# Performance work log

Measured on AMD Instinct MI355X. Metric: run time of the kernel, lower is better.

## Reference

```python
import jax, jax.numpy as jnp
import numpy as np

N = 50000
IN_DIM = 1024
HID = 64
HEADS = 4
OUT_DIM = 128
NEG_SLOPE = 0.2


def setup_inputs() -> dict:
    key = jax.random.key(0)
    ks = jax.random.split(key, 10)
    x = jax.random.normal(ks[0], (N, IN_DIM), dtype=jnp.float32)
    edge_index = jax.random.randint(ks[1], (2, 800000), 0, N, dtype=jnp.int64)
    # GATConv 1: input_dim -> hidden_dim, heads=HEADS, concat=True
    W1 = jax.random.normal(ks[2], (IN_DIM, HEADS * HID), dtype=jnp.float32) * (1.0 / np.sqrt(IN_DIM))
    att_src1 = jax.random.normal(ks[3], (HEADS, HID), dtype=jnp.float32) * 0.1
    att_dst1 = jax.random.normal(ks[4], (HEADS, HID), dtype=jnp.float32) * 0.1
    b1 = jnp.zeros((HEADS * HID,), dtype=jnp.float32)
    # GATConv 2: hidden_dim*heads -> output_dim, heads=1, concat=False
    W2 = jax.random.normal(ks[5], (HEADS * HID, OUT_DIM), dtype=jnp.float32) * (1.0 / np.sqrt(HEADS * HID))
    att_src2 = jax.random.normal(ks[6], (1, OUT_DIM), dtype=jnp.float32) * 0.1
    att_dst2 = jax.random.normal(ks[7], (1, OUT_DIM), dtype=jnp.float32) * 0.1
    b2 = jnp.zeros((OUT_DIM,), dtype=jnp.float32)
    return {"x": x, "edge_index": edge_index, "W1": W1, "att_src1": att_src1,
            "att_dst1": att_dst1, "b1": b1, "W2": W2, "att_src2": att_src2,
            "att_dst2": att_dst2, "b2": b2}


def _gat_conv(x, src, dst, W, a_src, a_dst, b, heads, concat):
    # x: [N, F_in]; src/dst: [E'] (self-loops already included)
    n = x.shape[0]
    h = (x @ W).reshape(n, heads, -1)                 # [N, H, D]
    # per-node attention halves (PyG style)
    alpha_s = jnp.sum(h * a_src[None], axis=-1)       # [N, H]
    alpha_d = jnp.sum(h * a_dst[None], axis=-1)       # [N, H]
    e = jax.nn.leaky_relu(alpha_s[src] + alpha_d[dst], NEG_SLOPE)  # [E', H]
    # segment softmax over incoming edges of each destination node
    m = jax.ops.segment_max(e, dst, num_segments=n)   # [N, H]
    m = jnp.where(jnp.isfinite(m), m, 0.0)
    e = jnp.exp(e - m[dst])
    s = jax.ops.segment_sum(e, dst, num_segments=n)   # [N, H]
    alpha = e / (s[dst] + 1e-16)                      # [E', H]
    out = jax.ops.segment_sum(h[src] * alpha[:, :, None], dst, num_segments=n)  # [N, H, D]
    out = out.reshape(n, -1) if concat else out.mean(axis=1)
    return out + b


def reference(x, edge_index, W1, att_src1, att_dst1, b1, W2, att_src2, att_dst2, b2):
    n = x.shape[0]
    # PyG GATConv default: add self-loops
    loops = jnp.arange(n, dtype=edge_index.dtype)
    src = jnp.concatenate([edge_index[0], loops])
    dst = jnp.concatenate([edge_index[1], loops])
    # dropout layers are identity in eval mode
    h = _gat_conv(x, src, dst, W1, att_src1, att_dst1, b1, HEADS, concat=True)
    h = jax.nn.elu(h)
    out = _gat_conv(h, src, dst, W2, att_src2, att_dst2, b2, 1, concat=False)
    # F.normalize(p=2, dim=-1)
    norm = jnp.maximum(jnp.linalg.norm(out, axis=-1, keepdims=True), 1e-12)
    return out / norm
```

## Files before the change

### kernel.cpp

```cpp
#include <hip/hip_runtime.h>
#include <math.h>

#define NNODES 50000
#define E0 800000
#define ETOT 850000
#define IN_DIM 1024
#define HEADS 4
#define C1 256
#define C2 128
#define NEG_SLOPE 0.2f

typedef short bf16x8 __attribute__((ext_vector_type(8)));
typedef float f32x4 __attribute__((ext_vector_type(4)));
typedef unsigned short ushort_t;

__device__ __forceinline__ void edge_sd(const int* __restrict__ ei, int e, int& s, int& d) {
    if (e < E0) { s = ei[e]; d = ei[E0 + e]; }
    else        { s = e - E0; d = s; }
}

__device__ __forceinline__ ushort_t f2b(float f) {
    unsigned u = __float_as_uint(f);
    return (ushort_t)((u + 0x7fffu + ((u >> 16) & 1u)) >> 16);
}
__device__ __forceinline__ float bf2f(ushort_t u) {
    return __uint_as_float((unsigned)u << 16);
}
__device__ __forceinline__ float lrelu(float v) { return v > 0.f ? v : NEG_SLOPE * v; }

__device__ __forceinline__ void gload_lds16(const void* g, void* l) {
    __builtin_amdgcn_global_load_lds(
        (const __attribute__((address_space(1))) unsigned int*)g,
        (__attribute__((address_space(3))) unsigned int*)l, 16, 0, 0);
}

__global__ __launch_bounds__(256) void wtrans_kernel(const float* __restrict__ W,
                                                     ushort_t* __restrict__ WT,
                                                     int K, int N)
{
    int idx = blockIdx.x * 256 + threadIdx.x;
    if (idx >= K * N) return;
    int k = idx / N, n = idx % N;
    WT[(size_t)n * K + k] = f2b(W[idx]);
}

__global__ __launch_bounds__(256) void gemm_fb(const float* __restrict__ A,
                                               const ushort_t* __restrict__ Bt,
                                               ushort_t* __restrict__ Cb,
                                               int M, int N, int K)
{
    __shared__ __align__(16) ushort_t As[4 * 128 * 8];
    __shared__ __align__(16) ushort_t Bs[4 * 128 * 8];

    const int tid  = threadIdx.x;
    const int lane = tid & 63;
    const int wid  = tid >> 6;
    const int wr   = wid >> 1, wc = wid & 1;
    const int rowBase = blockIdx.y * 128;
    const int colBase = blockIdx.x * 128;

    const int arow = tid >> 1;
    const int akh  = (tid & 1) * 2;
    const int aGRow = min(rowBase + arow, M - 1);
    const float* aptr = A + (size_t)aGRow * K + akh * 8;
    ushort_t* awr0 = &As[akh * 1024 + arow * 8];
    ushort_t* awr1 = awr0 + 1024;

    const ushort_t* bptr = Bt + (size_t)(colBase + lane) * K + wid * 8;
    ushort_t* bwr0 = &Bs[wid * 1024];
    ushort_t* bwr1 = bwr0 + 512;

    const int r0 = lane & 15;
    const int kh = lane >> 4;
    const ushort_t* ard = &As[kh * 1024 + (wr * 64 + r0) * 8];
    const ushort_t* brd = &Bs[kh * 1024 + (wc * 64 + r0) * 8];

    f32x4 zero = {0.f, 0.f, 0.f, 0.f};
    f32x4 acc[4][4];
    #pragma unroll
    for (int i = 0; i < 4; ++i)
        #pragma unroll
        for (int j = 0; j < 4; ++j) acc[i][j] = zero;

    for (int kt = 0; kt < K; kt += 32) {
        float4 f0 = *(const float4*)(aptr + kt + 0);
        float4 f1 = *(const float4*)(aptr + kt + 4);
        float4 f2 = *(const float4*)(aptr + kt + 8);
        float4 f3 = *(const float4*)(aptr + kt + 12);
        bf16x8 p0, p1;
        p0[0] = f2b(f0.x); p0[1] = f2b(f0.y); p0[2] = f2b(f0.z); p0[3] = f2b(f0.w);
        p0[4] = f2b(f1.x); p0[5] = f2b(f1.y); p0[6] = f2b(f1.z); p0[7] = f2b(f1.w);
        p1[0] = f2b(f2.x); p1[1] = f2b(f2.y); p1[2] = f2b(f2.z); p1[3] = f2b(f2.w);
        p1[4] = f2b(f3.x); p1[5] = f2b(f3.y); p1[6] = f2b(f3.z); p1[7] = f2b(f3.w);

        __syncthreads();
        *(bf16x8*)awr0 = p0;
        *(bf16x8*)awr1 = p1;
        gload_lds16(bptr + kt, bwr0);
        gload_lds16(bptr + (size_t)64 * K + kt, bwr1);
        __syncthreads();

        bf16x8 af[4], bfr[4];
        #pragma unroll
        for (int fi = 0; fi < 4; ++fi) af[fi] = *(const bf16x8*)(ard + fi * 128);
        #pragma unroll
        for (int fj = 0; fj < 4; ++fj) bfr[fj] = *(const bf16x8*)(brd + fj * 128);
        #pragma unroll
        for (int fi = 0; fi < 4; ++fi)
            #pragma unroll
            for (int fj = 0; fj < 4; ++fj)
                acc[fi][fj] = __builtin_amdgcn_mfma_f32_16x16x32_bf16(
                    af[fi], bfr[fj], acc[fi][fj], 0, 0, 0);
    }

    #pragma unroll
    for (int fi = 0; fi < 4; ++fi) {
        int row0 = rowBase + wr * 64 + fi * 16 + kh * 4;
        #pragma unroll
        for (int i = 0; i < 4; ++i) {
            int row = row0 + i;
            if (row < M) {
                #pragma unroll
                for (int fj = 0; fj < 4; ++fj)
                    Cb[(size_t)row * N + colBase + wc * 64 + fj * 16 + r0] = f2b(acc[fi][fj][i]);
            }
        }
    }
}

__global__ __launch_bounds__(256) void gemm_bb(const ushort_t* __restrict__ Ab,
                                               const ushort_t* __restrict__ Bt,
                                               ushort_t* __restrict__ Cb,
                                               int M, int N, int K)
{
    __shared__ __align__(16) ushort_t As[4 * 128 * 8];
    __shared__ __align__(16) ushort_t Bs[4 * 128 * 8];

    const int tid  = threadIdx.x;
    const int lane = tid & 63;
    const int wid  = tid >> 6;
    const int wr   = wid >> 1, wc = wid & 1;
    const int rowBase = blockIdx.y * 128;
    const int colBase = blockIdx.x * 128;

    const ushort_t* aptr0 = Ab + (size_t)min(rowBase + lane, M - 1) * K + wid * 8;
    const ushort_t* aptr1 = Ab + (size_t)min(rowBase + 64 + lane, M - 1) * K + wid * 8;
    ushort_t* awr0 = &As[wid * 1024];
    ushort_t* awr1 = awr0 + 512;

    const ushort_t* bptr = Bt + (size_t)(colBase + lane) * K + wid * 8;
    ushort_t* bwr0 = &Bs[wid * 1024];
    ushort_t* bwr1 = bwr0 + 512;

    const int r0 = lane & 15;
    const int kh = lane >> 4;
    const ushort_t* ard = &As[kh * 1024 + (wr * 64 + r0) * 8];
    const ushort_t* brd = &Bs[kh * 1024 + (wc * 64 + r0) * 8];

    f32x4 zero = {0.f, 0.f, 0.f, 0.f};
    f32x4 acc[4][4];
    #pragma unroll
    for (int i = 0; i < 4; ++i)
        #pragma unroll
        for (int j = 0; j < 4; ++j) acc[i][j] = zero;

    for (int kt = 0; kt < K; kt += 32) {
        __syncthreads();
        gload_lds16(aptr0 + kt, awr0);
        gload_lds16(aptr1 + kt, awr1);
        gload_lds16(bptr + kt, bwr0);
        gload_lds16(bptr + (size_t)64 * K + kt, bwr1);
        __syncthreads();

        bf16x8 af[4], bfr[4];
        #pragma unroll
        for (int fi = 0; fi < 4; ++fi) af[fi] = *(const bf16x8*)(ard + fi * 128);
        #pragma unroll
        for (int fj = 0; fj < 4; ++fj) bfr[fj] = *(const bf16x8*)(brd + fj * 128);
        #pragma unroll
        for (int fi = 0; fi < 4; ++fi)
            #pragma unroll
            for (int fj = 0; fj < 4; ++fj)
                acc[fi][fj] = __builtin_amdgcn_mfma_f32_16x16x32_bf16(
                    af[fi], bfr[fj], acc[fi][fj], 0, 0, 0);
    }

    #pragma unroll
    for (int fi = 0; fi < 4; ++fi) {
        int row0 = rowBase + wr * 64 + fi * 16 + kh * 4;
        #pragma unroll
        for (int i = 0; i < 4; ++i) {
            int row = row0 + i;
            if (row < M) {
                #pragma unroll
                for (int fj = 0; fj < 4; ++fj)
                    Cb[(size_t)row * N + colBase + wc * 64 + fj * 16 + r0] = f2b(acc[fi][fj][i]);
            }
        }
    }
}

__global__ __launch_bounds__(256) void alpha1_kernel(const ushort_t* __restrict__ h1b,
                                                     const float* __restrict__ asrc,
                                                     const float* __restrict__ adst,
                                                     float* __restrict__ out_s,
                                                     float* __restrict__ out_d)
{
    int n = blockIdx.x;
    int t = threadIdx.x;
    float h = bf2f(h1b[(size_t)n * C1 + t]);
    float s = h * asrc[t];
    float d = h * adst[t];
    #pragma unroll
    for (int off = 32; off > 0; off >>= 1) {
        s += __shfl_down(s, off);
        d += __shfl_down(d, off);
    }
    if ((t & 63) == 0) {
        out_s[n * HEADS + (t >> 6)] = s;
        out_d[n * HEADS + (t >> 6)] = d;
    }
}

__global__ __launch_bounds__(64) void alpha2_kernel(const ushort_t* __restrict__ h2b,
                                                    const float* __restrict__ asrc,
                                                    const float* __restrict__ adst,
                                                    float* __restrict__ out_s,
                                                    float* __restrict__ out_d)
{
    int n = blockIdx.x;
    int t = threadIdx.x;
    float a = bf2f(h2b[(size_t)n * C2 + t]);
    float b = bf2f(h2b[(size_t)n * C2 + t + 64]);
    float s = a * asrc[t] + b * asrc[t + 64];
    float d = a * adst[t] + b * adst[t + 64];
    #pragma unroll
    for (int off = 32; off > 0; off >>= 1) {
        s += __shfl_down(s, off);
        d += __shfl_down(d, off);
    }
    if (t == 0) { out_s[n] = s; out_d[n] = d; }
}

__global__ __launch_bounds__(256) void deg_kernel(const int* __restrict__ ei,
                                                  int* __restrict__ deg)
{
    int e = blockIdx.x * blockDim.x + threadIdx.x;
    if (e >= ETOT) return;
    int s, d; edge_sd(ei, e, s, d);
    atomicAdd(&deg[d], 1);
}

#define SCAN_T 1024
__global__ __launch_bounds__(SCAN_T) void scan_kernel(const int* __restrict__ deg,
                                                      int* __restrict__ rowptr)
{
    __shared__ int wsum[16];
    __shared__ int chunk_tot;
    __shared__ int carry_s;
    const int t = threadIdx.x, lane = t & 63, w = t >> 6;
    if (t == 0) carry_s = 0;
    __syncthreads();
    for (int base = 0; base < NNODES; base += SCAN_T * 4) {
        int idx = base + t * 4;
        int v0 = (idx + 0 < NNODES) ? deg[idx + 0] : 0;
        int v1 = (idx + 1 < NNODES) ? deg[idx + 1] : 0;
        int v2 = (idx + 2 < NNODES) ? deg[idx + 2] : 0;
        int v3 = (idx + 3 < NNODES) ? deg[idx + 3] : 0;
        int p0 = v0, p1 = p0 + v1, p2 = p1 + v2, p3 = p2 + v3;
        int incl = p3;
        #pragma unroll
        for (int off = 1; off < 64; off <<= 1) {
            int nb = __shfl_up(incl, off);
            if (lane >= off) incl += nb;
        }
        if (lane == 63) wsum[w] = incl;
        __syncthreads();
        if (w == 0 && lane < 16) {
            int ws = wsum[lane];
            int wincl = ws;
            #pragma unroll
            for (int off = 1; off < 16; off <<= 1) {
                int nb = __shfl_up(wincl, off);
                if (lane >= off) wincl += nb;
            }
            wsum[lane] = wincl - ws;
            if (lane == 15) chunk_tot = wincl;
        }
        __syncthreads();
        int carry = carry_s;
        int basev = carry + wsum[w] + (incl - p3);
        if (idx + 0 < NNODES) rowptr[idx + 0] = basev;
        if (idx + 1 < NNODES) rowptr[idx + 1] = basev + p0;
        if (idx + 2 < NNODES) rowptr[idx + 2] = basev + p1;
        if (idx + 3 < NNODES) rowptr[idx + 3] = basev + p2;
        __syncthreads();
        if (t == 0) carry_s = carry + chunk_tot;
        __syncthreads();
    }
    if (threadIdx.x == 0) rowptr[NNODES] = carry_s;
}

__global__ __launch_bounds__(256) void scatter_kernel(const int* __restrict__ ei,
                                                      int* __restrict__ cursor,
                                                      int* __restrict__ srcs)
{
    int e = blockIdx.x * blockDim.x + threadIdx.x;
    if (e >= ETOT) return;
    int s, d; edge_sd(ei, e, s, d);
    int pos = atomicAdd(&cursor[d], 1);
    srcs[pos] = s;
}

__global__ __launch_bounds__(256) void weights1_kernel(const int* __restrict__ rowptr,
                                                       const int* __restrict__ srcs,
                                                       const float4* __restrict__ as1,
                                                       const float4* __restrict__ ad1,
                                                       float4* __restrict__ wbuf)
{
    int d = blockIdx.x * 4 + (threadIdx.x >> 6);
    if (d >= NNODES) return;
    int lane = threadIdx.x & 63;
    int beg = rowptr[d], end = rowptr[d + 1];
    float4 adv = ad1[d];
    float m0 = -INFINITY, m1 = -INFINITY, m2 = -INFINITY, m3 = -INFINITY;
    for (int i = beg + lane; i < end; i += 64) {
        int s = srcs[i];
        float4 av = as1[s];
        m0 = fmaxf(m0, lrelu(av.x + adv.x));
        m1 = fmaxf(m1, lrelu(av.y + adv.y));
        m2 = fmaxf(m2, lrelu(av.z + adv.z));
        m3 = fmaxf(m3, lrelu(av.w + adv.w));
    }
    #pragma unroll
    for (int off = 32; off > 0; off >>= 1) {
        m0 = fmaxf(m0, __shfl_xor(m0, off));
        m1 = fmaxf(m1, __shfl_xor(m1, off));
        m2 = fmaxf(m2, __shfl_xor(m2, off));
        m3 = fmaxf(m3, __shfl_xor(m3, off));
    }
    float s0 = 0.f, s1 = 0.f, s2 = 0.f, s3 = 0.f;
    for (int i = beg + lane; i < end; i += 64) {
        int s = srcs[i];
        float4 av = as1[s];
        float w0 = expf(lrelu(av.x + adv.x) - m0);
        float w1 = expf(lrelu(av.y + adv.y) - m1);
        float w2 = expf(lrelu(av.z + adv.z) - m2);
        float w3 = expf(lrelu(av.w + adv.w) - m3);
        wbuf[i] = make_float4(w0, w1, w2, w3);
        s0 += w0; s1 += w1; s2 += w2; s3 += w3;
    }
    #pragma unroll
    for (int off = 32; off > 0; off >>= 1) {
        s0 += __shfl_xor(s0, off);
        s1 += __shfl_xor(s1, off);
        s2 += __shfl_xor(s2, off);
        s3 += __shfl_xor(s3, off);
    }
    float i0 = 1.f / (s0 + 1e-16f), i1 = 1.f / (s1 + 1e-16f);
    float i2 = 1.f / (s2 + 1e-16f), i3 = 1.f / (s3 + 1e-16f);
    for (int i = beg + lane; i < end; i += 64) {
        float4 wv = wbuf[i];
        wbuf[i] = make_float4(wv.x * i0, wv.y * i1, wv.z * i2, wv.w * i3);
    }
}

__global__ __launch_bounds__(256) void weights2_kernel(const int* __restrict__ rowptr,
                                                       const int* __restrict__ srcs,
                                                       const float* __restrict__ as2,
                                                       const float* __restrict__ ad2,
                                                       float* __restrict__ wbuf)
{
    int d = blockIdx.x * 4 + (threadIdx.x >> 6);
    if (d >= NNODES) return;
    int lane = threadIdx.x & 63;
    int beg = rowptr[d], end = rowptr[d + 1];
    float adv = ad2[d];
    float m = -INFINITY;
    for (int i = beg + lane; i < end; i += 64)
        m = fmaxf(m, lrelu(as2[srcs[i]] + adv));
    #pragma unroll
    for (int off = 32; off > 0; off >>= 1) m = fmaxf(m, __shfl_xor(m, off));
    float sm = 0.f;
    for (int i = beg + lane; i < end; i += 64) {
        float w = expf(lrelu(as2[srcs[i]] + adv) - m);
        wbuf[i] = w;
        sm += w;
    }
    #pragma unroll
    for (int off = 32; off > 0; off >>= 1) sm += __shfl_xor(sm, off);
    float inv = 1.f / (sm + 1e-16f);
    for (int i = beg + lane; i < end; i += 64) wbuf[i] *= inv;
}

__global__ __launch_bounds__(256) void aggr1_csr(const int* __restrict__ rowptr,
                                                 const int* __restrict__ srcs,
                                                 const ushort_t* __restrict__ h1b,
                                                 const float* __restrict__ wbuf,
                                                 const float* __restrict__ b1,
                                                 ushort_t* __restrict__ out)
{
    int d = blockIdx.x;
    int t = threadIdx.x;
    int head = t >> 6;
    int beg = rowptr[d], end = rowptr[d + 1];
    float acc = 0.f;
    int i = beg;
    for (; i + 1 < end; i += 2) {
        int s0 = srcs[i], s1 = srcs[i + 1];
        float a0 = wbuf[i * 4 + head], a1 = wbuf[i * 4 + 4 + head];
        float v0 = bf2f(h1b[(size_t)s0 * C1 + t]);
        float v1 = bf2f(h1b[(size_t)s1 * C1 + t]);
        acc = fmaf(a0, v0, acc);
        acc = fmaf(a1, v1, acc);
    }
    if (i < end) {
        int s0 = srcs[i];
        acc = fmaf(wbuf[i * 4 + head], bf2f(h1b[(size_t)s0 * C1 + t]), acc);
    }
    float o = acc + b1[t];
    out[(size_t)d * C1 + t] = f2b(o > 0.f ? o : (expf(o) - 1.f));
}

__global__ __launch_bounds__(128) void aggr2_csr(const int* __restrict__ rowptr,
                                                 const int* __restrict__ srcs,
                                                 const ushort_t* __restrict__ h2b,
                                                 const float* __restrict__ wbuf,
                                                 const float* __restrict__ b2,
                                                 float* __restrict__ out)
{
    int d = blockIdx.x;
    int t = threadIdx.x;
    int beg = rowptr[d], end = rowptr[d + 1];
    float acc = 0.f;
    int i = beg;
    for (; i + 1 < end; i += 2) {
        int s0 = srcs[i], s1 = srcs[i + 1];
        float a0 = wbuf[i], a1 = wbuf[i + 1];
        float v0 = bf2f(h2b[(size_t)s0 * C2 + t]);
        float v1 = bf2f(h2b[(size_t)s1 * C2 + t]);
        acc = fmaf(a0, v0, acc);
        acc = fmaf(a1, v1, acc);
    }
    if (i < end) acc = fmaf(wbuf[i], bf2f(h2b[(size_t)srcs[i] * C2 + t]), acc);
    float o = acc + b2[t];
    __shared__ float red[2];
    float sq = o * o;
    #pragma unroll
    for (int off = 32; off > 0; off >>= 1) sq += __shfl_down(sq, off);
    if ((t & 63) == 0) red[t >> 6] = sq;
    __syncthreads();
    float total = red[0] + red[1];
    float inv = 1.0f / fmaxf(sqrtf(total), 1e-12f);
    out[(size_t)d * C2 + t] = o * inv;
}

extern "C" void kernel_launch(void* const* d_in, const int* in_sizes, int n_in,
                              void* d_out, int out_size, void* d_ws, size_t ws_size,
                              hipStream_t stream)
{
    const float* x     = (const float*)d_in[0];
    const int*   ei    = (const int*)d_in[1];
    const float* W1    = (const float*)d_in[2];
    const float* asrc1 = (const float*)d_in[3];
    const float* adst1 = (const float*)d_in[4];
    const float* b1    = (const float*)d_in[5];
    const float* W2    = (const float*)d_in[6];
    const float* asrc2 = (const float*)d_in[7];
    const float* adst2 = (const float*)d_in[8];
    const float* b2    = (const float*)d_in[9];
    float* out = (float*)d_out;

    char* ws = (char*)d_ws;
    size_t off = 0;
    auto alloc = [&](size_t nbytes) {
        void* p = ws + off;
        off += (nbytes + 15) & ~(size_t)15;
        return p;
    };
    ushort_t* h1b    = (ushort_t*)alloc((size_t)NNODES * C1 * 2);
    ushort_t* act1b  = (ushort_t*)alloc((size_t)NNODES * C1 * 2);
    ushort_t* h2b    = (ushort_t*)alloc((size_t)NNODES * C2 * 2);
    ushort_t* W1T    = (ushort_t*)alloc((size_t)C1 * IN_DIM * 2);
    ushort_t* W2T    = (ushort_t*)alloc((size_t)C2 * C1 * 2);
    float*    as1    = (float*)alloc((size_t)NNODES * HEADS * 4);
    float*    ad1    = (float*)alloc((size_t)NNODES * HEADS * 4);
    float*    as2    = (float*)alloc((size_t)NNODES * 4);
    float*    ad2    = (float*)alloc((size_t)NNODES * 4);
    float*    wbuf1  = (float*)alloc((size_t)ETOT * HEADS * 4);
    float*    wbuf2  = (float*)alloc((size_t)ETOT * 4);
    int*      deg    = (int*)alloc((size_t)NNODES * 4);
    int*      rowptr = (int*)alloc((size_t)(NNODES + 1) * 4);
    int*      cursor = (int*)alloc((size_t)(NNODES + 1) * 4);
    int*      srcs   = (int*)alloc((size_t)ETOT * 4);

    const int eb = (ETOT + 255) / 256;
    const int nb4 = (NNODES + 3) / 4;

    wtrans_kernel<<<(IN_DIM * C1 + 255) / 256, 256, 0, stream>>>(W1, W1T, IN_DIM, C1);
    wtrans_kernel<<<(C1 * C2 + 255) / 256, 256, 0, stream>>>(W2, W2T, C1, C2);

    hipMemsetAsync(deg, 0, (size_t)NNODES * 4, stream);
    deg_kernel<<<eb, 256, 0, stream>>>(ei, deg);
    scan_kernel<<<1, SCAN_T, 0, stream>>>(deg, rowptr);
    hipMemcpyAsync(cursor, rowptr, (size_t)(NNODES + 1) * 4, hipMemcpyDeviceToDevice, stream);
    scatter_kernel<<<eb, 256, 0, stream>>>(ei, cursor, srcs);

    dim3 g1(C1 / 128, (NNODES + 127) / 128);
    gemm_fb<<<g1, 256, 0, stream>>>(x, W1T, h1b, NNODES, C1, IN_DIM);
    alpha1_kernel<<<NNODES, 256, 0, stream>>>(h1b, asrc1, adst1, as1, ad1);
    weights1_kernel<<<nb4, 256, 0, stream>>>(rowptr, srcs, (const float4*)as1,
                                             (const float4*)ad1, (float4*)wbuf1);
    aggr1_csr<<<NNODES, 256, 0, stream>>>(rowptr, srcs, h1b, wbuf1, b1, act1b);

    dim3 g2(C2 / 128, (NNODES + 127) / 128);
    gemm_bb<<<g2, 256, 0, stream>>>(act1b, W2T, h2b, NNODES, C2, C1);
    alpha2_kernel<<<NNODES, 64, 0, stream>>>(h2b, asrc2, adst2, as2, ad2);
    weights2_kernel<<<nb4, 256, 0, stream>>>(rowptr, srcs, as2, ad2, wbuf2);
    aggr2_csr<<<NNODES, 128, 0, stream>>>(rowptr, srcs, h2b, wbuf2, b2, out);
}
```

Baseline: 535.4 us.

## Double-buffer LDS tiles in both GEMM kernels to overlap loads with MFMA

Both GEMM kernels now keep two LDS buffers per operand. The next K-tile is prefetched into the idle buffer while MFMAs run on the current one, so each iteration needs one barrier instead of two. Launch bounds gain occupancy hints (3 and 4 blocks per CU). In exchange the kernels use twice the LDS and more registers, since the fp32 A prefetch values stay live across the MFMA block, which may cut occupancy.

```diff
diff --git a/kernel.cpp b/kernel.cpp
--- a/kernel.cpp
+++ b/kernel.cpp
@@ -44,13 +44,13 @@
     WT[(size_t)n * K + k] = f2b(W[idx]);
 }
 
-__global__ __launch_bounds__(256) void gemm_fb(const float* __restrict__ A,
-                                               const ushort_t* __restrict__ Bt,
-                                               ushort_t* __restrict__ Cb,
-                                               int M, int N, int K)
-{
-    __shared__ __align__(16) ushort_t As[4 * 128 * 8];
-    __shared__ __align__(16) ushort_t Bs[4 * 128 * 8];
+__global__ __launch_bounds__(256, 3) void gemm_fb(const float* __restrict__ A,
+                                                  const ushort_t* __restrict__ Bt,
+                                                  ushort_t* __restrict__ Cb,
+                                                  int M, int N, int K)
+{
+    __shared__ __align__(16) ushort_t As[2][4 * 128 * 8];
+    __shared__ __align__(16) ushort_t Bs[2][4 * 128 * 8];
 
     const int tid  = threadIdx.x;
     const int lane = tid & 63;
@@ -63,17 +63,17 @@
     const int akh  = (tid & 1) * 2;
     const int aGRow = min(rowBase + arow, M - 1);
     const float* aptr = A + (size_t)aGRow * K + akh * 8;
-    ushort_t* awr0 = &As[akh * 1024 + arow * 8];
-    ushort_t* awr1 = awr0 + 1024;
+    const int awoff0 = akh * 1024 + arow * 8;
+    const int awoff1 = awoff0 + 1024;
 
     const ushort_t* bptr = Bt + (size_t)(colBase + lane) * K + wid * 8;
-    ushort_t* bwr0 = &Bs[wid * 1024];
-    ushort_t* bwr1 = bwr0 + 512;
+    const int bwoff0 = wid * 1024;
+    const int bwoff1 = bwoff0 + 512;
 
     const int r0 = lane & 15;
     const int kh = lane >> 4;
-    const ushort_t* ard = &As[kh * 1024 + (wr * 64 + r0) * 8];
-    const ushort_t* brd = &Bs[kh * 1024 + (wc * 64 + r0) * 8];
+    const int ardoff = kh * 1024 + (wr * 64 + r0) * 8;
+    const int brdoff = kh * 1024 + (wc * 64 + r0) * 8;
 
     f32x4 zero = {0.f, 0.f, 0.f, 0.f};
     f32x4 acc[4][4];
@@ -82,35 +82,64 @@
         #pragma unroll
         for (int j = 0; j < 4; ++j) acc[i][j] = zero;
 
-    for (int kt = 0; kt < K; kt += 32) {
-        float4 f0 = *(const float4*)(aptr + kt + 0);
-        float4 f1 = *(const float4*)(aptr + kt + 4);
-        float4 f2 = *(const float4*)(aptr + kt + 8);
-        float4 f3 = *(const float4*)(aptr + kt + 12);
+    {
+        float4 f0 = *(const float4*)(aptr + 0);
+        float4 f1 = *(const float4*)(aptr + 4);
+        float4 f2 = *(const float4*)(aptr + 8);
+        float4 f3 = *(const float4*)(aptr + 12);
         bf16x8 p0, p1;
         p0[0] = f2b(f0.x); p0[1] = f2b(f0.y); p0[2] = f2b(f0.z); p0[3] = f2b(f0.w);
         p0[4] = f2b(f1.x); p0[5] = f2b(f1.y); p0[6] = f2b(f1.z); p0[7] = f2b(f1.w);
         p1[0] = f2b(f2.x); p1[1] = f2b(f2.y); p1[2] = f2b(f2.z); p1[3] = f2b(f2.w);
         p1[4] = f2b(f3.x); p1[5] = f2b(f3.y); p1[6] = f2b(f3.z); p1[7] = f2b(f3.w);
-
-        __syncthreads();
-        *(bf16x8*)awr0 = p0;
-        *(bf16x8*)awr1 = p1;
-        gload_lds16(bptr + kt, bwr0);
-        gload_lds16(bptr + (size_t)64 * K + kt, bwr1);
-        __syncthreads();
+        *(bf16x8*)&As[0][awoff0] = p0;
+        *(bf16x8*)&As[0][awoff1] = p1;
+        gload_lds16(bptr, &Bs[0][bwoff0]);
+        gload_lds16(bptr + (size_t)64 * K, &Bs[0][bwoff1]);
+    }
+    __syncthreads();
+
+    const ushort_t* rdA = As[0]; const ushort_t* rdB = Bs[0];
+    ushort_t*       stA = As[1]; ushort_t*       stB = Bs[1];
+
+    const int nt = K >> 5;
+    for (int t = 0; t < nt; ++t) {
+        const int kt = (t + 1) << 5;
+        const bool has_next = kt < K;
+        float4 f0, f1, f2, f3;
+        if (has_next) {
+            gload_lds16(bptr + kt, stB + bwoff0);
+            gload_lds16(bptr + (size_t)64 * K + kt, stB + bwoff1);
+            f0 = *(const float4*)(aptr + kt + 0);
+            f1 = *(const float4*)(aptr + kt + 4);
+            f2 = *(const float4*)(aptr + kt + 8);
+            f3 = *(const float4*)(aptr + kt + 12);
+        }
 
         bf16x8 af[4], bfr[4];
         #pragma unroll
-        for (int fi = 0; fi < 4; ++fi) af[fi] = *(const bf16x8*)(ard + fi * 128);
-        #pragma unroll
-        for (int fj = 0; fj < 4; ++fj) bfr[fj] = *(const bf16x8*)(brd + fj * 128);
+        for (int fi = 0; fi < 4; ++fi) af[fi] = *(const bf16x8*)(rdA + ardoff + fi * 128);
+        #pragma unroll
+        for (int fj = 0; fj < 4; ++fj) bfr[fj] = *(const bf16x8*)(rdB + brdoff + fj * 128);
         #pragma unroll
         for (int fi = 0; fi < 4; ++fi)
             #pragma unroll
             for (int fj = 0; fj < 4; ++fj)
                 acc[fi][fj] = __builtin_amdgcn_mfma_f32_16x16x32_bf16(
                     af[fi], bfr[fj], acc[fi][fj], 0, 0, 0);
+
+        if (has_next) {
+            bf16x8 p0, p1;
+            p0[0] = f2b(f0.x); p0[1] = f2b(f0.y); p0[2] = f2b(f0.z); p0[3] = f2b(f0.w);
+            p0[4] = f2b(f1.x); p0[5] = f2b(f1.y); p0[6] = f2b(f1.z); p0[7] = f2b(f1.w);
+            p1[0] = f2b(f2.x); p1[1] = f2b(f2.y); p1[2] = f2b(f2.z); p1[3] = f2b(f2.w);
+            p1[4] = f2b(f3.x); p1[5] = f2b(f3.y); p1[6] = f2b(f3.z); p1[7] = f2b(f3.w);
+            *(bf16x8*)(stA + awoff0) = p0;
+            *(bf16x8*)(stA + awoff1) = p1;
+        }
+        __syncthreads();
+        const ushort_t* tA = rdA; rdA = stA; stA = (ushort_t*)tA;
+        const ushort_t* tB = rdB; rdB = stB; stB = (ushort_t*)tB;
     }
 
     #pragma unroll
@@ -128,13 +157,13 @@
     }
 }
 
-__global__ __launch_bounds__(256) void gemm_bb(const ushort_t* __restrict__ Ab,
-                                               const ushort_t* __restrict__ Bt,
-                                               ushort_t* __restrict__ Cb,
-                                               int M, int N, int K)
-{
-    __shared__ __align__(16) ushort_t As[4 * 128 * 8];
-    __shared__ __align__(16) ushort_t Bs[4 * 128 * 8];
+__global__ __launch_bounds__(256, 4) void gemm_bb(const ushort_t* __restrict__ Ab,
+                                                  const ushort_t* __restrict__ Bt,
+                                                  ushort_t* __restrict__ Cb,
+                                                  int M, int N, int K)
+{
+    __shared__ __align__(16) ushort_t As[2][4 * 128 * 8];
+    __shared__ __align__(16) ushort_t Bs[2][4 * 128 * 8];
 
     const int tid  = threadIdx.x;
     const int lane = tid & 63;
@@ -145,17 +174,14 @@
 
     const ushort_t* aptr0 = Ab + (size_t)min(rowBase + lane, M - 1) * K + wid * 8;
     const ushort_t* aptr1 = Ab + (size_t)min(rowBase + 64 + lane, M - 1) * K + wid * 8;
-    ushort_t* awr0 = &As[wid * 1024];
-    ushort_t* awr1 = awr0 + 512;
-
-    const ushort_t* bptr = Bt + (size_t)(colBase + lane) * K + wid * 8;
-    ushort_t* bwr0 = &Bs[wid * 1024];
-    ushort_t* bwr1 = bwr0 + 512;
+    const ushort_t* bptr  = Bt + (size_t)(colBase + lane) * K + wid * 8;
+    const int woff0 = wid * 1024;
+    const int woff1 = woff0 + 512;
 
     const int r0 = lane & 15;
     const int kh = lane >> 4;
-    const ushort_t* ard = &As[kh * 1024 + (wr * 64 + r0) * 8];
-    const ushort_t* brd = &Bs[kh * 1024 + (wc * 64 + r0) * 8];
+    const int ardoff = kh * 1024 + (wr * 64 + r0) * 8;
+    const int brdoff = kh * 1024 + (wc * 64 + r0) * 8;
 
     f32x4 zero = {0.f, 0.f, 0.f, 0.f};
     f32x4 acc[4][4];
@@ -164,25 +190,40 @@
         #pragma unroll
         for (int j = 0; j < 4; ++j) acc[i][j] = zero;
 
-    for (int kt = 0; kt < K; kt += 32) {
-        __syncthreads();
-        gload_lds16(aptr0 + kt, awr0);
-        gload_lds16(aptr1 + kt, awr1);
-        gload_lds16(bptr + kt, bwr0);
-        gload_lds16(bptr + (size_t)64 * K + kt, bwr1);
-        __syncthreads();
+    gload_lds16(aptr0, &As[0][woff0]);
+    gload_lds16(aptr1, &As[0][woff1]);
+    gload_lds16(bptr,  &Bs[0][woff0]);
+    gload_lds16(bptr + (size_t)64 * K, &Bs[0][woff1]);
+    __syncthreads();
+
+    const ushort_t* rdA = As[0]; const ushort_t* rdB = Bs[0];
+    ushort_t*       stA = As[1]; ushort_t*       stB = Bs[1];
+
+    const int nt = K >> 5;
+    for (int t = 0; t < nt; ++t) {
+        const int kt = (t + 1) << 5;
+        if (kt < K) {
+            gload_lds16(aptr0 + kt, stA + woff0);
+            gload_lds16(aptr1 + kt, stA + woff1);
+            gload_lds16(bptr + kt,  stB + woff0);
+            gload_lds16(bptr + (size_t)64 * K + kt, stB + woff1);
+        }
 
         bf16x8 af[4], bfr[4];
         #pragma unroll
-        for (int fi = 0; fi < 4; ++fi) af[fi] = *(const bf16x8*)(ard + fi * 128);
-        #pragma unroll
-        for (int fj = 0; fj < 4; ++fj) bfr[fj] = *(const bf16x8*)(brd + fj * 128);
+        for (int fi = 0; fi < 4; ++fi) af[fi] = *(const bf16x8*)(rdA + ardoff + fi * 128);
+        #pragma unroll
+        for (int fj = 0; fj < 4; ++fj) bfr[fj] = *(const bf16x8*)(rdB + brdoff + fj * 128);
         #pragma unroll
         for (int fi = 0; fi < 4; ++fi)
             #pragma unroll
             for (int fj = 0; fj < 4; ++fj)
                 acc[fi][fj] = __builtin_amdgcn_mfma_f32_16x16x32_bf16(
                     af[fi], bfr[fj], acc[fi][fj], 0, 0, 0);
+
+        __syncthreads();
+        const ushort_t* tA = rdA; rdA = stA; stA = (ushort_t*)tA;
+        const ushort_t* tB = rdB; rdB = stB; stB = (ushort_t*)tB;
     }
 
     #pragma unroll
```

After: 539.5 us. Within noise of the previous version (+0.8%).
